# Kernel optimization log

Measured on AMD Instinct MI355X. Metric: run time of the kernel, lower is better.

Reference implementation:

```python
import jax, jax.numpy as jnp
import numpy as np

# Static conv config (matches init_kwargs)
KH, KW = 3, 3
PAD, STRIDE, DIL = 1, 1, 1


def _quantize_dynamic_int8_per_tensor(t):
    """Dynamic symmetric per-tensor int8 quantization: scale = absmax/127."""
    scale = jnp.max(jnp.abs(t)) / 127.0
    q = jnp.clip(jnp.round(t / scale), -128, 127).astype(jnp.int32)
    return q, scale


def _im2col(q, kh, kw, pad, stride, dil):
    """q: (B,C,H,W) int32 -> (B, OH*OW, C*kh*kw), torch im2col ordering (C slowest)."""
    B, C, H, W = q.shape
    OH = (H + 2 * pad - dil * (kh - 1) - 1) // stride + 1
    OW = (W + 2 * pad - dil * (kw - 1) - 1) // stride + 1
    qp = jnp.pad(q, ((0, 0), (0, 0), (pad, pad), (pad, pad)))
    row = jnp.arange(kh)[:, None] * dil + jnp.arange(OH)[None, :] * stride  # (kh, OH)
    col = jnp.arange(kw)[:, None] * dil + jnp.arange(OW)[None, :] * stride  # (kw, OW)
    # patches: (B, C, kh, kw, OH, OW)
    patches = qp[:, :, row[:, None, :, None], col[None, :, None, :]]
    patches = patches.reshape(B, C * kh * kw, OH * OW)
    return patches.transpose(0, 2, 1), OH, OW  # (B, L, C*kh*kw)


def reference(x, weight, bias, lut):
    B, C, H, W = x.shape
    O = weight.shape[0]
    # dynamic per-tensor int8 quantization of activations and weights
    qx, scale_x = _quantize_dynamic_int8_per_tensor(x)
    qw, scale_w = _quantize_dynamic_int8_per_tensor(weight)
    cols, OH, OW = _im2col(qx, KH, KW, PAD, STRIDE, DIL)  # (B, L, K)
    wmat = qw.reshape(O, -1)                               # (O, K)
    wi = wmat + 128                                        # LUT column index

    def bgemm_one(colb):  # colb: (L, K) -> (L, O) int32 via LUT multiply-accumulate
        vals = lut[colb[:, None, :] + 128, wi[None, :, :]]  # (L, O, K)
        return vals.sum(-1)

    out = jax.lax.map(bgemm_one, cols)                     # (B, L, O) int32
    out = out.astype(jnp.float32).transpose(0, 2, 1).reshape(B, O, OH, OW)
    out = out * scale_x * scale_w                          # dequantize
    out = out + bias[None, :, None, None]
    return out


def setup_inputs() -> dict:
    key = jax.random.key(0)
    k1, k2, k3 = jax.random.split(key, 3)
    x = jax.random.normal(k1, (4, 32, 32, 32), dtype=jnp.float32)
    weight = jax.random.normal(k2, (64, 32, 3, 3), dtype=jnp.float32) * 0.1
    bias = jax.random.normal(k3, (64,), dtype=jnp.float32)
    # LUT: approximate int8 multiply table indexed by (a+128, b+128).
    # Exact product table is a faithful instance of the abstraction.
    vals = np.arange(-128, 128, dtype=np.int32)
    lut = jnp.asarray(vals[:, None] * vals[None, :])  # (256, 256) int32
    return {"x": x, "weight": weight, "bias": bias, "lut": lut}
```

## Files before the change

### kernel.cpp

```cpp
#include <hip/hip_runtime.h>


#define BB   4
#define CC   32
#define HH   32
#define WW   32
#define OO   64
#define NX   (BB*CC*HH*WW)
#define NW   (OO*CC*3*3)

#define PART_N_X 64
#define PART_N_W 8
#define QXP_DW_OFF 128
#define QWP_DW_OFF (128 + 32768)

static __device__ inline unsigned wave_umax(unsigned m) {
    #pragma unroll
    for (int off = 32; off > 0; off >>= 1) {
        unsigned o = __shfl_down(m, off, 64);
        m = m > o ? m : o;
    }
    return m;
}

static __device__ inline int dot4(unsigned a, unsigned b, int c) {
#if __has_builtin(__builtin_amdgcn_sdot4)
    return __builtin_amdgcn_sdot4((int)a, (int)b, c, false);
#else
    c += (int)(signed char)(a      ) * (int)(signed char)(b      );
    c += (int)(signed char)(a >> 8 ) * (int)(signed char)(b >> 8 );
    c += (int)(signed char)(a >> 16) * (int)(signed char)(b >> 16);
    c += (int)(signed char)(a >> 24) * (int)(signed char)(b >> 24);
    return c;
#endif
}

static __device__ inline unsigned absbits(float f) {
    return __float_as_uint(f) & 0x7fffffffu;
}

__global__ __launch_bounds__(256) void absmax_part(const float* __restrict__ x,
                                                   const float* __restrict__ w,
                                                   unsigned* __restrict__ part) {
    int bid = blockIdx.x, tid = threadIdx.x;
    unsigned m = 0u;
    if (bid < 64) {
        const float4* p = (const float4*)x;
        int base = bid * 512;
        #pragma unroll
        for (int i = 0; i < 2; ++i) {
            float4 v = p[base + tid + i * 256];
            m = max(m, max(max(absbits(v.x), absbits(v.y)),
                           max(absbits(v.z), absbits(v.w))));
        }
    } else {
        const float4* p = (const float4*)w;
        int base = (bid - 64) * 576;
        for (int i = tid; i < 576; i += 256) {
            float4 v = p[base + i];
            m = max(m, max(max(absbits(v.x), absbits(v.y)),
                           max(absbits(v.z), absbits(v.w))));
        }
    }
    __shared__ unsigned sred[4];
    m = wave_umax(m);
    if ((tid & 63) == 0) sred[tid >> 6] = m;
    __syncthreads();
    if (tid == 0)
        part[bid] = max(max(sred[0], sred[1]), max(sred[2], sred[3]));
}

__global__ __launch_bounds__(256) void quant_pack(const float* __restrict__ x,
                                                  const float* __restrict__ w,
                                                  const unsigned* __restrict__ part,
                                                  unsigned* __restrict__ qxp,
                                                  unsigned* __restrict__ qwp) {
    int bid = blockIdx.x, tid = threadIdx.x;
    bool isx = bid < 128;
    __shared__ float ssc;
    {
        unsigned v = 0u;
        if (isx) { if (tid < PART_N_X) v = part[tid]; }
        else     { if (tid < PART_N_W) v = part[64 + tid]; }
        if (tid < 64) {
            unsigned m = wave_umax(v);
            if (tid == 0) ssc = __uint_as_float(m) / 127.0f;
        }
    }
    __syncthreads();
    float scale = ssc;

    if (isx) {
        int d = bid * 256 + tid;
        int b   = d >> 13;
        int rem = d & 8191;
        int c4  = rem >> 10;
        int p   = rem & 1023;
        const float* src = x + (b * 32 + c4 * 4) * 1024 + p;
        unsigned pk = 0u;
        #pragma unroll
        for (int j = 0; j < 4; ++j) {
            float q = rintf(src[j * 1024] / scale);
            q = fminf(fmaxf(q, -128.0f), 127.0f);
            int qi = (int)q;
            pk |= ((unsigned)(qi & 0xff)) << (8 * j);
        }
        qxp[d] = pk;
    } else {
        int idx = (bid - 128) * 256 + tid;
        int o  = idx / 72;
        int r  = idx - o * 72;
        int c4 = r / 9;
        int kk = r - c4 * 9;
        const float* src = w + o * 288 + (c4 * 4) * 9 + kk;
        unsigned pk = 0u;
        #pragma unroll
        for (int j = 0; j < 4; ++j) {
            float q = rintf(src[j * 9] / scale);
            q = fminf(fmaxf(q, -128.0f), 127.0f);
            int qi = (int)q;
            pk |= ((unsigned)(qi & 0xff)) << (8 * j);
        }
        qwp[idx] = pk;
    }
}

__global__ __launch_bounds__(256) void conv3(const unsigned* __restrict__ qxp,
                                             const unsigned* __restrict__ qwp,
                                             const float* __restrict__ bias,
                                             const unsigned* __restrict__ part,
                                             float* __restrict__ out) {
    int bid = blockIdx.x, tid = threadIdx.x;
    int og = bid & 15;
    int rt = (bid >> 4) & 3;
    int b  = bid >> 6;

    __shared__ unsigned xls[8 * 10 * 34];
    __shared__ float scl[2];

    {
        unsigned v = 0u;
        if (tid < PART_N_X) v = part[tid];
        else if (tid >= 64 && tid < 64 + PART_N_W) v = part[64 + (tid - 64)];
        if (tid < 128) {
            unsigned m = wave_umax(v);
            if ((tid & 63) == 0) scl[tid >> 6] = __uint_as_float(m) / 127.0f;
        }
    }

    for (int i = tid; i < 2720; i += 256) {
        int c4  = i / 340;
        int rem = i - c4 * 340;
        int rr  = rem / 34;
        int col = rem - rr * 34;
        int ih = rt * 8 + rr - 1;
        int iw = col - 1;
        unsigned val = 0u;
        if ((unsigned)ih < 32u && (unsigned)iw < 32u)
            val = qxp[((b * 8 + c4) * 32 + ih) * 32 + iw];
        xls[i] = val;
    }
    __syncthreads();

    float sx = scl[0], sw = scl[1];
    int r  = tid >> 5;
    int ow = tid & 31;

    int acc0 = 0, acc1 = 0, acc2 = 0, acc3 = 0;
    const unsigned* wp = qwp + og * 4 * 72;

    #pragma unroll
    for (int c4 = 0; c4 < 8; ++c4) {
        #pragma unroll
        for (int kh = 0; kh < 3; ++kh) {
            const unsigned* xrow = &xls[(c4 * 10 + r + kh) * 34 + ow];
            unsigned x0 = xrow[0], x1 = xrow[1], x2 = xrow[2];
            int wb = c4 * 9 + kh * 3;
            acc0 = dot4(x0, wp[0 * 72 + wb + 0], acc0);
            acc0 = dot4(x1, wp[0 * 72 + wb + 1], acc0);
            acc0 = dot4(x2, wp[0 * 72 + wb + 2], acc0);
            acc1 = dot4(x0, wp[1 * 72 + wb + 0], acc1);
            acc1 = dot4(x1, wp[1 * 72 + wb + 1], acc1);
            acc1 = dot4(x2, wp[1 * 72 + wb + 2], acc1);
            acc2 = dot4(x0, wp[2 * 72 + wb + 0], acc2);
            acc2 = dot4(x1, wp[2 * 72 + wb + 1], acc2);
            acc2 = dot4(x2, wp[2 * 72 + wb + 2], acc2);
            acc3 = dot4(x0, wp[3 * 72 + wb + 0], acc3);
            acc3 = dot4(x1, wp[3 * 72 + wb + 1], acc3);
            acc3 = dot4(x2, wp[3 * 72 + wb + 2], acc3);
        }
    }

    int oh = rt * 8 + r;
    int acc[4] = {acc0, acc1, acc2, acc3};
    #pragma unroll
    for (int oo = 0; oo < 4; ++oo) {
        int o = og * 4 + oo;
        float v = ((float)acc[oo] * sx) * sw + bias[o];
        out[((b * 64 + o) * 32 + oh) * 32 + ow] = v;
    }
}

extern "C" void kernel_launch(void* const* d_in, const int* in_sizes, int n_in,
                              void* d_out, int out_size, void* d_ws, size_t ws_size,
                              hipStream_t stream) {
    const float* x      = (const float*)d_in[0];
    const float* weight = (const float*)d_in[1];
    const float* bias   = (const float*)d_in[2];

    unsigned* ws32 = (unsigned*)d_ws;
    unsigned* part = ws32;
    unsigned* qxp  = ws32 + QXP_DW_OFF;
    unsigned* qwp  = ws32 + QWP_DW_OFF;
    float* out = (float*)d_out;

    absmax_part<<<72, 256, 0, stream>>>(x, weight, part);
    quant_pack<<<146, 256, 0, stream>>>(x, weight, part, qxp, qwp);
    conv3<<<256, 256, 0, stream>>>(qxp, qwp, bias, part, out);
}
```

Baseline: 71.85 us.

## Fuse quantize-pack into conv kernel, quantizing tiles on the fly into LDS

Removes the separate quant_pack kernel and its intermediate int8-packed buffers. The conv kernel now reads float activations and weights directly, quantizes and packs them into shared memory (including a new weight tile in LDS), then runs the dot4 loop. This drops one kernel launch and a global round trip. In exchange, halo rows and weights are re-quantized redundantly across blocks, and each block reads four times more bytes as floats.

After: 77.09 us. 1.07x slower.

```diff
diff --git a/kernel.cpp b/kernel.cpp
--- a/kernel.cpp
+++ b/kernel.cpp
@@ -1,18 +1,8 @@
 #include <hip/hip_runtime.h>
 
 
-#define BB   4
-#define CC   32
-#define HH   32
-#define WW   32
-#define OO   64
-#define NX   (BB*CC*HH*WW)
-#define NW   (OO*CC*3*3)
-
 #define PART_N_X 64
 #define PART_N_W 8
-#define QXP_DW_OFF 128
-#define QWP_DW_OFF (128 + 32768)
 
 static __device__ inline unsigned wave_umax(unsigned m) {
     #pragma unroll
@@ -37,6 +27,17 @@
 
 static __device__ inline unsigned absbits(float f) {
     return __float_as_uint(f) & 0x7fffffffu;
+}
+
+static __device__ inline unsigned quant_pack4(const float* src, int stride, float scale) {
+    unsigned pk = 0u;
+    #pragma unroll
+    for (int j = 0; j < 4; ++j) {
+        float q = rintf(src[j * stride] / scale);
+        q = fminf(fmaxf(q, -128.0f), 127.0f);
+        pk |= ((unsigned)((int)q & 0xff)) << (8 * j);
+    }
+    return pk;
 }
 
 __global__ __launch_bounds__(256) void absmax_part(const float* __restrict__ x,
@@ -70,72 +71,18 @@
         part[bid] = max(max(sred[0], sred[1]), max(sred[2], sred[3]));
 }
 
-__global__ __launch_bounds__(256) void quant_pack(const float* __restrict__ x,
+__global__ __launch_bounds__(256) void conv_fused(const float* __restrict__ x,
                                                   const float* __restrict__ w,
+                                                  const float* __restrict__ bias,
                                                   const unsigned* __restrict__ part,
-                                                  unsigned* __restrict__ qxp,
-                                                  unsigned* __restrict__ qwp) {
-    int bid = blockIdx.x, tid = threadIdx.x;
-    bool isx = bid < 128;
-    __shared__ float ssc;
-    {
-        unsigned v = 0u;
-        if (isx) { if (tid < PART_N_X) v = part[tid]; }
-        else     { if (tid < PART_N_W) v = part[64 + tid]; }
-        if (tid < 64) {
-            unsigned m = wave_umax(v);
-            if (tid == 0) ssc = __uint_as_float(m) / 127.0f;
-        }
-    }
-    __syncthreads();
-    float scale = ssc;
-
-    if (isx) {
-        int d = bid * 256 + tid;
-        int b   = d >> 13;
-        int rem = d & 8191;
-        int c4  = rem >> 10;
-        int p   = rem & 1023;
-        const float* src = x + (b * 32 + c4 * 4) * 1024 + p;
-        unsigned pk = 0u;
-        #pragma unroll
-        for (int j = 0; j < 4; ++j) {
-            float q = rintf(src[j * 1024] / scale);
-            q = fminf(fmaxf(q, -128.0f), 127.0f);
-            int qi = (int)q;
-            pk |= ((unsigned)(qi & 0xff)) << (8 * j);
-        }
-        qxp[d] = pk;
-    } else {
-        int idx = (bid - 128) * 256 + tid;
-        int o  = idx / 72;
-        int r  = idx - o * 72;
-        int c4 = r / 9;
-        int kk = r - c4 * 9;
-        const float* src = w + o * 288 + (c4 * 4) * 9 + kk;
-        unsigned pk = 0u;
-        #pragma unroll
-        for (int j = 0; j < 4; ++j) {
-            float q = rintf(src[j * 9] / scale);
-            q = fminf(fmaxf(q, -128.0f), 127.0f);
-            int qi = (int)q;
-            pk |= ((unsigned)(qi & 0xff)) << (8 * j);
-        }
-        qwp[idx] = pk;
-    }
-}
-
-__global__ __launch_bounds__(256) void conv3(const unsigned* __restrict__ qxp,
-                                             const unsigned* __restrict__ qwp,
-                                             const float* __restrict__ bias,
-                                             const unsigned* __restrict__ part,
-                                             float* __restrict__ out) {
+                                                  float* __restrict__ out) {
     int bid = blockIdx.x, tid = threadIdx.x;
     int og = bid & 15;
     int rt = (bid >> 4) & 3;
     int b  = bid >> 6;
 
     __shared__ unsigned xls[8 * 10 * 34];
+    __shared__ unsigned wls[4 * 72];
     __shared__ float scl[2];
 
     {
@@ -147,6 +94,17 @@
             if ((tid & 63) == 0) scl[tid >> 6] = __uint_as_float(m) / 127.0f;
         }
     }
+    __syncthreads();
+    float sx = scl[0], sw = scl[1];
+
+    for (int i = tid; i < 288; i += 256) {
+        int o  = i / 72;
+        int r  = i - o * 72;
+        int c4 = r / 9;
+        int kk = r - c4 * 9;
+        const float* src = w + (og * 4 + o) * 288 + (c4 * 4) * 9 + kk;
+        wls[i] = quant_pack4(src, 9, sw);
+    }
 
     for (int i = tid; i < 2720; i += 256) {
         int c4  = i / 340;
@@ -156,18 +114,17 @@
         int ih = rt * 8 + rr - 1;
         int iw = col - 1;
         unsigned val = 0u;
-        if ((unsigned)ih < 32u && (unsigned)iw < 32u)
-            val = qxp[((b * 8 + c4) * 32 + ih) * 32 + iw];
+        if ((unsigned)ih < 32u && (unsigned)iw < 32u) {
+            const float* src = x + ((b * 32 + c4 * 4) * 32 + ih) * 32 + iw;
+            val = quant_pack4(src, 1024, sx);
+        }
         xls[i] = val;
     }
     __syncthreads();
 
-    float sx = scl[0], sw = scl[1];
     int r  = tid >> 5;
     int ow = tid & 31;
-
     int acc0 = 0, acc1 = 0, acc2 = 0, acc3 = 0;
-    const unsigned* wp = qwp + og * 4 * 72;
 
     #pragma unroll
     for (int c4 = 0; c4 < 8; ++c4) {
@@ -176,18 +133,18 @@
             const unsigned* xrow = &xls[(c4 * 10 + r + kh) * 34 + ow];
             unsigned x0 = xrow[0], x1 = xrow[1], x2 = xrow[2];
             int wb = c4 * 9 + kh * 3;
-            acc0 = dot4(x0, wp[0 * 72 + wb + 0], acc0);
-            acc0 = dot4(x1, wp[0 * 72 + wb + 1], acc0);
-            acc0 = dot4(x2, wp[0 * 72 + wb + 2], acc0);
-            acc1 = dot4(x0, wp[1 * 72 + wb + 0], acc1);
-            acc1 = dot4(x1, wp[1 * 72 + wb + 1], acc1);
-            acc1 = dot4(x2, wp[1 * 72 + wb + 2], acc1);
-            acc2 = dot4(x0, wp[2 * 72 + wb + 0], acc2);
-            acc2 = dot4(x1, wp[2 * 72 + wb + 1], acc2);
-            acc2 = dot4(x2, wp[2 * 72 + wb + 2], acc2);
-            acc3 = dot4(x0, wp[3 * 72 + wb + 0], acc3);
-            acc3 = dot4(x1, wp[3 * 72 + wb + 1], acc3);
-            acc3 = dot4(x2, wp[3 * 72 + wb + 2], acc3);
+            acc0 = dot4(x0, wls[0 * 72 + wb + 0], acc0);
+            acc0 = dot4(x1, wls[0 * 72 + wb + 1], acc0);
+            acc0 = dot4(x2, wls[0 * 72 + wb + 2], acc0);
+            acc1 = dot4(x0, wls[1 * 72 + wb + 0], acc1);
+            acc1 = dot4(x1, wls[1 * 72 + wb + 1], acc1);
+            acc1 = dot4(x2, wls[1 * 72 + wb + 2], acc1);
+            acc2 = dot4(x0, wls[2 * 72 + wb + 0], acc2);
+            acc2 = dot4(x1, wls[2 * 72 + wb + 1], acc2);
+            acc2 = dot4(x2, wls[2 * 72 + wb + 2], acc2);
+            acc3 = dot4(x0, wls[3 * 72 + wb + 0], acc3);
+            acc3 = dot4(x1, wls[3 * 72 + wb + 1], acc3);
+            acc3 = dot4(x2, wls[3 * 72 + wb + 2], acc3);
         }
     }
 
@@ -208,13 +165,9 @@
     const float* weight = (const float*)d_in[1];
     const float* bias   = (const float*)d_in[2];
 
-    unsigned* ws32 = (unsigned*)d_ws;
-    unsigned* part = ws32;
-    unsigned* qxp  = ws32 + QXP_DW_OFF;
-    unsigned* qwp  = ws32 + QWP_DW_OFF;
+    unsigned* part = (unsigned*)d_ws;
     float* out = (float*)d_out;
 
     absmax_part<<<72, 256, 0, stream>>>(x, weight, part);
-    quant_pack<<<146, 256, 0, stream>>>(x, weight, part, qxp, qwp);
-    conv3<<<256, 256, 0, stream>>>(qxp, qwp, bias, part, out);
+    conv_fused<<<256, 256, 0, stream>>>(x, weight, bias, part, out);
 }
```
